# Performance work log

Hardware: AMD Instinct MI355X
Metric: run time of the kernel (lower is better)

The kernel has to match this reference:

```python
import jax, jax.numpy as jnp
import numpy as np

N = 30000      # nodes
E = 480000     # edges (before self loops)
C = 64         # in_channels
L = 32         # latent_dim
H = 2          # heads
SLOPE = 0.2    # PyG GATConv default negative_slope


def _param(key, shape, fan_in):
    return jax.random.normal(key, shape, jnp.float32) * (1.0 / np.sqrt(fan_in))


def setup_inputs() -> dict:
    key = jax.random.key(0)
    ks = jax.random.split(key, 32)
    d = {
        "x": jax.random.normal(ks[0], (N, C), jnp.float32),
        "edge_index": jax.random.randint(ks[1], (2, E), 0, N),
        "use_neighbors": 1,
        # GATConv params: W [heads*out, in], att_src/att_dst [heads, out], bias [heads*out]
        # encoder_conv1: in=C, out=2C, heads=H
        "W1": _param(ks[2], (H * 2 * C, C), C),
        "as1": _param(ks[3], (H, 2 * C), 2 * C),
        "ad1": _param(ks[4], (H, 2 * C), 2 * C),
        "b1": jnp.zeros((H * 2 * C,), jnp.float32),
        # encoder_conv2: in=2C*H, out=L, heads=1
        "W2": _param(ks[5], (L, 2 * C * H), 2 * C * H),
        "as2": _param(ks[6], (1, L), L),
        "ad2": _param(ks[7], (1, L), L),
        "b2": jnp.zeros((L,), jnp.float32),
        # decoder_conv1: in=L, out=2C, heads=H
        "W3": _param(ks[8], (H * 2 * C, L), L),
        "as3": _param(ks[9], (H, 2 * C), 2 * C),
        "ad3": _param(ks[10], (H, 2 * C), 2 * C),
        "b3": jnp.zeros((H * 2 * C,), jnp.float32),
        # decoder_conv2: in=2C*H, out=C, heads=1
        "W4": _param(ks[11], (C, 2 * C * H), 2 * C * H),
        "as4": _param(ks[12], (1, C), C),
        "ad4": _param(ks[13], (1, C), C),
        "b4": jnp.zeros((C,), jnp.float32),
        # dense (non-neighbor) branch Linear params [out, in] + bias
        "el1w": _param(ks[14], (2 * C, C), C), "el1b": jnp.zeros((2 * C,), jnp.float32),
        "el2w": _param(ks[15], (L, 2 * C), 2 * C), "el2b": jnp.zeros((L,), jnp.float32),
        "dl1w": _param(ks[16], (2 * C, L), L), "dl1b": jnp.zeros((2 * C,), jnp.float32),
        "dl2w": _param(ks[17], (C, 2 * C), 2 * C), "dl2b": jnp.zeros((C,), jnp.float32),
    }
    return d


def gat_conv(x, src, dst, W, att_src, att_dst, bias, heads, out_ch):
    """PyG GATConv (concat=True, self loops already in src/dst)."""
    n = x.shape[0]
    h = (x @ W.T).reshape(n, heads, out_ch)            # [N,H,F]
    a_s = jnp.sum(h * att_src[None], -1)               # [N,H]
    a_d = jnp.sum(h * att_dst[None], -1)               # [N,H]
    e = jax.nn.leaky_relu(a_s[src] + a_d[dst], SLOPE)  # [Etot,H]
    m = jax.ops.segment_max(e, dst, num_segments=n)
    ex = jnp.exp(e - m[dst])
    den = jax.ops.segment_sum(ex, dst, num_segments=n)
    alpha = ex / den[dst]                              # segment softmax over incoming edges
    msg = h[src] * alpha[..., None]                    # [Etot,H,F]
    out = jax.ops.segment_sum(msg, dst, num_segments=n)
    return out.reshape(n, heads * out_ch) + bias


def reference(x, edge_index, use_neighbors,
              W1, as1, ad1, b1, W2, as2, ad2, b2,
              W3, as3, ad3, b3, W4, as4, ad4, b4,
              el1w, el1b, el2w, el2b, dl1w, dl1b, dl2w, dl2b):
    if use_neighbors:
        loops = jnp.arange(N)
        src = jnp.concatenate([edge_index[0], loops])
        dst = jnp.concatenate([edge_index[1], loops])
        h = jax.nn.relu(gat_conv(x, src, dst, W1, as1, ad1, b1, H, 2 * C))
        z = gat_conv(h, src, dst, W2, as2, ad2, b2, 1, L)
        h = jax.nn.relu(gat_conv(z, src, dst, W3, as3, ad3, b3, H, 2 * C))
        return gat_conv(h, src, dst, W4, as4, ad4, b4, 1, C)
    else:
        h = jax.nn.relu(x @ el1w.T + el1b)
        z = h @ el2w.T + el2b
        h = jax.nn.relu(z @ dl1w.T + dl1b)
        return h @ dl2w.T + dl2b
```

## Files before the change

### kernel.cpp

```cpp
#include <hip/hip_runtime.h>
#include <hip/hip_bf16.h>
#include <math.h>

#define NODES 30000
#define WAVE 64
#define SCAN_T 1024
#define SCAN_CH 32
#define SCAN_CAP (SCAN_T * SCAN_CH)

static __device__ __forceinline__ float lrelu(float x) {
    return (x > 0.f) ? x : 0.2f * x;
}

__global__ __launch_bounds__(256) void gemm_xwt(
    const float* __restrict__ X, int lda, const float* __restrict__ W,
    const float* __restrict__ bias, float* __restrict__ out, int ldc,
    int Nrows, int M, int K, int relu,
    const float* __restrict__ att_s, const float* __restrict__ att_d,
    float* __restrict__ as_out, float* __restrict__ ad_out,
    const int* __restrict__ flag, int wantFlag)
{
    if (((*flag != 0) ? 1 : 0) != wantFlag) return;

    const int z = blockIdx.z;
    X += (size_t)z * K;
    W += (size_t)z * M * K;
    if (bias) bias += (size_t)z * M;
    out += (size_t)z * M;

    __shared__ float As[16][68];
    __shared__ float Bs[16][68];

    const int t  = threadIdx.x;
    const int tx = t & 15;
    const int ty = t >> 4;
    const int rowBase = blockIdx.y * 64;
    const int colBase = blockIdx.x * 64;

    float acc[4][4];
#pragma unroll
    for (int i = 0; i < 4; i++)
#pragma unroll
        for (int j = 0; j < 4; j++) acc[i][j] = 0.f;

    const int r_ld = t >> 2;
    const int k_ld = (t & 3) * 4;

    for (int kt = 0; kt < K; kt += 16) {
        float4 av = make_float4(0.f, 0.f, 0.f, 0.f);
        int grow = rowBase + r_ld;
        if (grow < Nrows)
            av = *reinterpret_cast<const float4*>(&X[(size_t)grow * lda + kt + k_ld]);
        As[k_ld + 0][r_ld] = av.x;
        As[k_ld + 1][r_ld] = av.y;
        As[k_ld + 2][r_ld] = av.z;
        As[k_ld + 3][r_ld] = av.w;
        float4 bv = make_float4(0.f, 0.f, 0.f, 0.f);
        int gm = colBase + r_ld;
        if (gm < M)
            bv = *reinterpret_cast<const float4*>(&W[(size_t)gm * K + kt + k_ld]);
        Bs[k_ld + 0][r_ld] = bv.x;
        Bs[k_ld + 1][r_ld] = bv.y;
        Bs[k_ld + 2][r_ld] = bv.z;
        Bs[k_ld + 3][r_ld] = bv.w;
        __syncthreads();

#pragma unroll
        for (int kk = 0; kk < 16; ++kk) {
            const float4 a = *reinterpret_cast<const float4*>(&As[kk][ty * 4]);
            const float4 b = *reinterpret_cast<const float4*>(&Bs[kk][tx * 4]);
            acc[0][0] += a.x * b.x; acc[0][1] += a.x * b.y; acc[0][2] += a.x * b.z; acc[0][3] += a.x * b.w;
            acc[1][0] += a.y * b.x; acc[1][1] += a.y * b.y; acc[1][2] += a.y * b.z; acc[1][3] += a.y * b.w;
            acc[2][0] += a.z * b.x; acc[2][1] += a.z * b.y; acc[2][2] += a.z * b.z; acc[2][3] += a.z * b.w;
            acc[3][0] += a.w * b.x; acc[3][1] += a.w * b.y; acc[3][2] += a.w * b.z; acc[3][3] += a.w * b.w;
        }
        __syncthreads();
    }

    const int col0 = colBase + tx * 4;
#pragma unroll
    for (int i = 0; i < 4; i++) {
        int row = rowBase + ty * 4 + i;
        if (row >= Nrows) continue;
        if (col0 >= M) continue;
        float4 v = make_float4(acc[i][0], acc[i][1], acc[i][2], acc[i][3]);
        if (bias) {
            v.x += bias[col0 + 0]; v.y += bias[col0 + 1];
            v.z += bias[col0 + 2]; v.w += bias[col0 + 3];
        }
        if (relu) {
            v.x = fmaxf(v.x, 0.f); v.y = fmaxf(v.y, 0.f);
            v.z = fmaxf(v.z, 0.f); v.w = fmaxf(v.w, 0.f);
        }
        *reinterpret_cast<float4*>(&out[(size_t)row * ldc + col0]) = v;
    }

    if (att_s) {
        float4 asv = make_float4(0.f, 0.f, 0.f, 0.f), adv = asv;
        if (col0 < M) {
            asv = *reinterpret_cast<const float4*>(&att_s[col0]);
            adv = *reinterpret_cast<const float4*>(&att_d[col0]);
        }
#pragma unroll
        for (int i = 0; i < 4; i++) {
            float ps = acc[i][0] * asv.x + acc[i][1] * asv.y + acc[i][2] * asv.z + acc[i][3] * asv.w;
            float pd = acc[i][0] * adv.x + acc[i][1] * adv.y + acc[i][2] * adv.z + acc[i][3] * adv.w;
#pragma unroll
            for (int off = 8; off; off >>= 1) {
                ps += __shfl_xor(ps, off);
                pd += __shfl_xor(pd, off);
            }
            int row = rowBase + ty * 4 + i;
            if (tx == 0 && row < Nrows) {
                as_out[row] = ps;
                ad_out[row] = pd;
            }
        }
    }
}

template <int HH, int F, int K>
__global__ __launch_bounds__(256) void fold_att(
    const float* __restrict__ W, const float* __restrict__ as_,
    const float* __restrict__ ad_, float* __restrict__ us,
    float* __restrict__ ud, const int* __restrict__ flag)
{
    if (*flag == 0) return;
    const int b   = blockIdx.x;
    const int sel = b / HH;
    const int h   = b % HH;
    const float* att = sel ? ad_ : as_;
    float* uo = sel ? ud : us;

    constexpr int NG = 256 / K;
    const int k  = threadIdx.x % K;
    const int fg = threadIdx.x / K;

    float s = 0.f;
#pragma unroll
    for (int f = fg; f < F; f += NG)
        s += att[h * F + f] * W[(size_t)(h * F + f) * K + k];

    __shared__ float red[256];
    red[threadIdx.x] = s;
    __syncthreads();
    if (fg == 0) {
        float tot = s;
#pragma unroll
        for (int g = 1; g < NG; g++) tot += red[g * K + k];
        uo[h * K + k] = tot;
    }
}

template <int K, int HH>
__global__ __launch_bounds__(256) void att_from_x(
    const float* __restrict__ xin, const float* __restrict__ us,
    const float* __restrict__ ud, float* __restrict__ as_out,
    float* __restrict__ ad_out, const int* __restrict__ flag)
{
    if (*flag == 0) return;
    constexpr int NPW = WAVE / K;
    const int wid  = threadIdx.x >> 6;
    const int lane = threadIdx.x & 63;
    const int sub  = lane / K;
    const int col  = lane % K;
    const int node = (blockIdx.x * 4 + wid) * NPW + sub;

    float v = 0.f;
    if (node < NODES) v = xin[(size_t)node * K + col];
    float ps[HH], pd[HH];
#pragma unroll
    for (int h = 0; h < HH; h++) {
        ps[h] = v * us[h * K + col];
        pd[h] = v * ud[h * K + col];
    }
#pragma unroll
    for (int off = K / 2; off; off >>= 1) {
#pragma unroll
        for (int h = 0; h < HH; h++) {
            ps[h] += __shfl_xor(ps[h], off);
            pd[h] += __shfl_xor(pd[h], off);
        }
    }
    if (col == 0 && node < NODES) {
#pragma unroll
        for (int h = 0; h < HH; h++) {
            as_out[node * HH + h] = ps[h];
            ad_out[node * HH + h] = pd[h];
        }
    }
}

template <int K, int HH>
__global__ __launch_bounds__(256) void gat_aggr_x(
    const float* __restrict__ xin, const float* __restrict__ as_,
    const float* __restrict__ ad_, const int* __restrict__ rowptr,
    const int* __restrict__ csr_src, float* __restrict__ agg,
    const int* __restrict__ flag)
{
    if (*flag == 0) return;
    const int node = blockIdx.x * 4 + (threadIdx.x >> 6);
    const int lane = threadIdx.x & 63;
    if (node >= NODES) return;

    const int beg = rowptr[node], end = rowptr[node + 1];
    const int deg = end - beg;

    float adv[HH];
#pragma unroll
    for (int h = 0; h < HH; h++) adv[h] = ad_[node * HH + h];

    float wl[HH];
    float mx[HH], rden[HH];
    const bool fast = (deg <= WAVE);

    if (fast) {
        float e[HH];
        int i = beg + lane;
        if (i < end) {
            int s = csr_src[i];
#pragma unroll
            for (int h = 0; h < HH; h++)
                e[h] = lrelu(as_[s * HH + h] + adv[h]);
        } else {
#pragma unroll
            for (int h = 0; h < HH; h++) e[h] = -1e30f;
        }
#pragma unroll
        for (int h = 0; h < HH; h++) {
            mx[h] = e[h];
#pragma unroll
            for (int off = 32; off; off >>= 1)
                mx[h] = fmaxf(mx[h], __shfl_xor(mx[h], off));
            float ex = __expf(e[h] - mx[h]);
            wl[h] = ex;
            float dn = ex;
#pragma unroll
            for (int off = 32; off; off >>= 1)
                dn += __shfl_xor(dn, off);
            rden[h] = 1.f / dn;
        }
    } else {
        float den[HH];
#pragma unroll
        for (int h = 0; h < HH; h++) { mx[h] = -1e30f; den[h] = 0.f; }
        for (int i = beg + lane; i < end; i += WAVE) {
            int s = csr_src[i];
#pragma unroll
            for (int h = 0; h < HH; h++)
                mx[h] = fmaxf(mx[h], lrelu(as_[s * HH + h] + adv[h]));
        }
#pragma unroll
        for (int h = 0; h < HH; h++)
#pragma unroll
            for (int off = 32; off; off >>= 1)
                mx[h] = fmaxf(mx[h], __shfl_xor(mx[h], off));
        for (int i = beg + lane; i < end; i += WAVE) {
            int s = csr_src[i];
#pragma unroll
            for (int h = 0; h < HH; h++)
                den[h] += __expf(lrelu(as_[s * HH + h] + adv[h]) - mx[h]);
        }
#pragma unroll
        for (int h = 0; h < HH; h++) {
#pragma unroll
            for (int off = 32; off; off >>= 1)
                den[h] += __shfl_xor(den[h], off);
            rden[h] = 1.f / den[h];
        }
    }

    constexpr int LPG = K / 4;
    constexpr int GR  = WAVE / LPG;
    const int esub = lane / LPG;
    const int c4   = lane % LPG;

    float4 acc[HH];
#pragma unroll
    for (int h = 0; h < HH; h++) acc[h] = make_float4(0.f, 0.f, 0.f, 0.f);

    if (fast) {
        const int iters = (deg + GR - 1) / GR;
        for (int it = 0; it < iters; ++it) {
            const int i = beg + it * GR + esub;
            const bool valid = (i < end);
            const int srcl = valid ? (i - beg) : 0;
            float w[HH];
#pragma unroll
            for (int h = 0; h < HH; h++)
                w[h] = __shfl(wl[h], srcl);
            if (valid) {
                int s = csr_src[i];
                float4 xv = *reinterpret_cast<const float4*>(&xin[(size_t)s * K + c4 * 4]);
#pragma unroll
                for (int h = 0; h < HH; h++) {
                    acc[h].x += xv.x * w[h];
                    acc[h].y += xv.y * w[h];
                    acc[h].z += xv.z * w[h];
                    acc[h].w += xv.w * w[h];
                }
            }
        }
    } else {
        for (int i = beg + esub; i < end; i += GR) {
            int s = csr_src[i];
            float w[HH];
#pragma unroll
            for (int h = 0; h < HH; h++)
                w[h] = __expf(lrelu(as_[s * HH + h] + adv[h]) - mx[h]);
            float4 xv = *reinterpret_cast<const float4*>(&xin[(size_t)s * K + c4 * 4]);
#pragma unroll
            for (int h = 0; h < HH; h++) {
                acc[h].x += xv.x * w[h];
                acc[h].y += xv.y * w[h];
                acc[h].z += xv.z * w[h];
                acc[h].w += xv.w * w[h];
            }
        }
    }
#pragma unroll
    for (int off = LPG; off < WAVE; off <<= 1) {
#pragma unroll
        for (int h = 0; h < HH; h++) {
            acc[h].x += __shfl_xor(acc[h].x, off);
            acc[h].y += __shfl_xor(acc[h].y, off);
            acc[h].z += __shfl_xor(acc[h].z, off);
            acc[h].w += __shfl_xor(acc[h].w, off);
        }
    }
    if (esub == 0) {
#pragma unroll
        for (int h = 0; h < HH; h++) {
            float4 o = make_float4(acc[h].x * rden[h], acc[h].y * rden[h],
                                   acc[h].z * rden[h], acc[h].w * rden[h]);
            *reinterpret_cast<float4*>(&agg[(size_t)node * (HH * K) + h * K + c4 * 4]) = o;
        }
    }
}

template <int HF, int RELU>
__global__ __launch_bounds__(256) void gat_aggr_h(
    const float* __restrict__ hsrc, const float* __restrict__ as_,
    const float* __restrict__ ad_, const int* __restrict__ rowptr,
    const int* __restrict__ csr_src, const float* __restrict__ bias,
    float* __restrict__ out, const int* __restrict__ flag)
{
    if (*flag == 0) return;
    const int node = blockIdx.x * 4 + (threadIdx.x >> 6);
    const int lane = threadIdx.x & 63;
    if (node >= NODES) return;

    const int beg = rowptr[node], end = rowptr[node + 1];
    const int deg = end - beg;
    const float adv = ad_[node];

    float wl, mx, rden;
    const bool fast = (deg <= WAVE);

    if (fast) {
        int i = beg + lane;
        float e = -1e30f;
        if (i < end) {
            int s = csr_src[i];
            e = lrelu(as_[s] + adv);
        }
        mx = e;
#pragma unroll
        for (int off = 32; off; off >>= 1)
            mx = fmaxf(mx, __shfl_xor(mx, off));
        wl = __expf(e - mx);
        float dn = wl;
#pragma unroll
        for (int off = 32; off; off >>= 1)
            dn += __shfl_xor(dn, off);
        rden = 1.f / dn;
    } else {
        mx = -1e30f;
        float den = 0.f;
        for (int i = beg + lane; i < end; i += WAVE) {
            int s = csr_src[i];
            mx = fmaxf(mx, lrelu(as_[s] + adv));
        }
#pragma unroll
        for (int off = 32; off; off >>= 1)
            mx = fmaxf(mx, __shfl_xor(mx, off));
        for (int i = beg + lane; i < end; i += WAVE) {
            int s = csr_src[i];
            den += __expf(lrelu(as_[s] + adv) - mx);
        }
#pragma unroll
        for (int off = 32; off; off >>= 1)
            den += __shfl_xor(den, off);
        rden = 1.f / den;
        wl = 0.f;
    }

    constexpr int LPG = HF / 4;
    constexpr int GR  = WAVE / LPG;
    const int esub = lane / LPG;
    const int c4   = lane % LPG;

    float4 acc = make_float4(0.f, 0.f, 0.f, 0.f);
    if (fast) {
        const int iters = (deg + GR - 1) / GR;
        for (int it = 0; it < iters; ++it) {
            const int i = beg + it * GR + esub;
            const bool valid = (i < end);
            const int srcl = valid ? (i - beg) : 0;
            float w = __shfl(wl, srcl);
            if (valid) {
                int s = csr_src[i];
                float4 hv = *reinterpret_cast<const float4*>(&hsrc[(size_t)s * HF + c4 * 4]);
                acc.x += hv.x * w; acc.y += hv.y * w; acc.z += hv.z * w; acc.w += hv.w * w;
            }
        }
    } else {
        for (int i = beg + esub; i < end; i += GR) {
            int s = csr_src[i];
            float w = __expf(lrelu(as_[s] + adv) - mx);
            float4 hv = *reinterpret_cast<const float4*>(&hsrc[(size_t)s * HF + c4 * 4]);
            acc.x += hv.x * w; acc.y += hv.y * w; acc.z += hv.z * w; acc.w += hv.w * w;
        }
    }
#pragma unroll
    for (int off = LPG; off < WAVE; off <<= 1) {
        acc.x += __shfl_xor(acc.x, off);
        acc.y += __shfl_xor(acc.y, off);
        acc.z += __shfl_xor(acc.z, off);
        acc.w += __shfl_xor(acc.w, off);
    }
    if (esub == 0) {
        float4 bv = *reinterpret_cast<const float4*>(&bias[c4 * 4]);
        float4 o = make_float4(acc.x * rden + bv.x, acc.y * rden + bv.y,
                               acc.z * rden + bv.z, acc.w * rden + bv.w);
        if (RELU) {
            o.x = fmaxf(o.x, 0.f); o.y = fmaxf(o.y, 0.f);
            o.z = fmaxf(o.z, 0.f); o.w = fmaxf(o.w, 0.f);
        }
        *reinterpret_cast<float4*>(&out[(size_t)node * HF + c4 * 4]) = o;
    }
}

__global__ void zero_int(int* __restrict__ p, int n, const int* __restrict__ flag)
{
    if (*flag == 0) return;
    for (int i = blockIdx.x * blockDim.x + threadIdx.x; i < n; i += gridDim.x * blockDim.x)
        p[i] = 0;
}

__global__ void count_deg(const int* __restrict__ ei, int* __restrict__ deg,
                          int E_, int Nn, const int* __restrict__ flag)
{
    if (*flag == 0) return;
    int e = blockIdx.x * blockDim.x + threadIdx.x;
    int tot = E_ + Nn;
    if (e >= tot) return;
    int dst = (e < E_) ? ei[E_ + e] : (e - E_);
    atomicAdd(&deg[dst], 1);
}

__global__ __launch_bounds__(SCAN_T) void scan_deg(
    const int* __restrict__ deg, int* __restrict__ rowptr,
    int* __restrict__ cursor, const int* __restrict__ flag)
{
    if (*flag == 0) return;
    __shared__ int sums[SCAN_T];
    const int t = threadIdx.x;
    const int base = t * SCAN_CH;

    int v[SCAN_CH];
    const int4* dp = reinterpret_cast<const int4*>(deg + base);
#pragma unroll
    for (int j = 0; j < SCAN_CH / 4; j++) {
        int4 q = dp[j];
        v[4 * j + 0] = q.x; v[4 * j + 1] = q.y;
        v[4 * j + 2] = q.z; v[4 * j + 3] = q.w;
    }
    int s = 0;
#pragma unroll
    for (int j = 0; j < SCAN_CH; j++) s += v[j];
    sums[t] = s;
    __syncthreads();
    for (int off = 1; off < SCAN_T; off <<= 1) {
        int x = (t >= off) ? sums[t - off] : 0;
        __syncthreads();
        sums[t] += x;
        __syncthreads();
    }
    int run = sums[t] - s;
    if (t == 0) rowptr[0] = 0;
#pragma unroll
    for (int j = 0; j < SCAN_CH; j++) {
        cursor[base + j] = run;
        run += v[j];
        rowptr[base + j + 1] = run;
    }
}

__global__ void scatter_edges(const int* __restrict__ ei, int* __restrict__ cursor,
                              int* __restrict__ csr_src, int E_, int Nn,
                              const int* __restrict__ flag)
{
    if (*flag == 0) return;
    int e = blockIdx.x * blockDim.x + threadIdx.x;
    int tot = E_ + Nn;
    if (e >= tot) return;
    int src, dst;
    if (e < E_) { src = ei[e]; dst = ei[E_ + e]; }
    else        { src = e - E_; dst = src; }
    int pos = atomicAdd(&cursor[dst], 1);
    csr_src[pos] = src;
}

extern "C" void kernel_launch(void* const* d_in, const int* in_sizes, int n_in,
                              void* d_out, int out_size, void* d_ws, size_t ws_size,
                              hipStream_t stream)
{
    const float* x    = (const float*)d_in[0];
    const int*   ei   = (const int*)d_in[1];
    const int*   flag = (const int*)d_in[2];
    const float* W1 = (const float*)d_in[3];
    const float* as1 = (const float*)d_in[4];
    const float* ad1 = (const float*)d_in[5];
    const float* b1 = (const float*)d_in[6];
    const float* W2 = (const float*)d_in[7];
    const float* as2 = (const float*)d_in[8];
    const float* ad2 = (const float*)d_in[9];
    const float* b2 = (const float*)d_in[10];
    const float* W3 = (const float*)d_in[11];
    const float* as3 = (const float*)d_in[12];
    const float* ad3 = (const float*)d_in[13];
    const float* b3 = (const float*)d_in[14];
    const float* W4 = (const float*)d_in[15];
    const float* as4 = (const float*)d_in[16];
    const float* ad4 = (const float*)d_in[17];
    const float* b4 = (const float*)d_in[18];
    const float* el1w = (const float*)d_in[19];
    const float* el1b = (const float*)d_in[20];
    const float* el2w = (const float*)d_in[21];
    const float* el2b = (const float*)d_in[22];
    const float* dl1w = (const float*)d_in[23];
    const float* dl1b = (const float*)d_in[24];
    const float* dl2w = (const float*)d_in[25];
    const float* dl2b = (const float*)d_in[26];

    const int E_   = in_sizes[1] / 2;
    const int Etot = E_ + NODES;

    char* base = (char*)d_ws;
    size_t off = 0;
    auto carve = [&](size_t bytes) -> void* {
        void* p = base + off;
        off = (off + bytes + 255) & ~(size_t)255;
        return p;
    };
    float* T0  = (float*)carve((size_t)NODES * 128 * 4);
    float* A   = (float*)carve((size_t)NODES * 256 * 4);
    float* T1  = (float*)carve((size_t)NODES * 64 * 4);
    float* Bz  = (float*)carve((size_t)NODES * 32 * 4);
    float* asb = (float*)carve((size_t)NODES * 2 * 4);
    float* adb = (float*)carve((size_t)NODES * 2 * 4);
    float* u1s = (float*)carve(2 * 64 * 4);
    float* u1d = (float*)carve(2 * 64 * 4);
    float* u3s = (float*)carve(2 * 32 * 4);
    float* u3d = (float*)carve(2 * 32 * 4);
    int* deg    = (int*)carve((size_t)SCAN_CAP * 4);
    int* rowptr = (int*)carve((size_t)(SCAN_CAP + 1) * 4);
    int* cursor = (int*)carve((size_t)SCAN_CAP * 4);
    int* csr    = (int*)carve((size_t)Etot * 4);
    (void)ws_size; (void)n_in; (void)out_size;

    float* outp = (float*)d_out;
    float* agg  = T0;

    const int nodeBlocks = (NODES + 3) / 4;
    const int edgeBlocks = (Etot + 255) / 256;
    dim3 blk(256);
    const int rowTiles = (NODES + 63) / 64;

    zero_int<<<(SCAN_CAP + 255) / 256, 256, 0, stream>>>(deg, SCAN_CAP, flag);
    count_deg<<<edgeBlocks, 256, 0, stream>>>(ei, deg, E_, NODES, flag);
    scan_deg<<<1, SCAN_T, 0, stream>>>(deg, rowptr, cursor, flag);
    scatter_edges<<<edgeBlocks, 256, 0, stream>>>(ei, cursor, csr, E_, NODES, flag);

    fold_att<2, 128, 64><<<4, 256, 0, stream>>>(W1, as1, ad1, u1s, u1d, flag);
    att_from_x<64, 2><<<nodeBlocks, blk, 0, stream>>>(x, u1s, u1d, asb, adb, flag);
    gat_aggr_x<64, 2><<<nodeBlocks, blk, 0, stream>>>(x, asb, adb, rowptr, csr, agg, flag);
    gemm_xwt<<<dim3(2, rowTiles, 2), blk, 0, stream>>>(agg, 128, W1, b1, A, 256, NODES, 128, 64, 1,
                                                       nullptr, nullptr, nullptr, nullptr, flag, 1);

    gemm_xwt<<<dim3(1, rowTiles, 1), blk, 0, stream>>>(A, 256, W2, nullptr, T1, 32, NODES, 32, 256, 0,
                                                       as2, ad2, asb, adb, flag, 1);
    gat_aggr_h<32, 0><<<nodeBlocks, blk, 0, stream>>>(T1, asb, adb, rowptr, csr, b2, Bz, flag);

    fold_att<2, 128, 32><<<4, 256, 0, stream>>>(W3, as3, ad3, u3s, u3d, flag);
    att_from_x<32, 2><<<(NODES + 7) / 8, blk, 0, stream>>>(Bz, u3s, u3d, asb, adb, flag);
    gat_aggr_x<32, 2><<<nodeBlocks, blk, 0, stream>>>(Bz, asb, adb, rowptr, csr, agg, flag);
    gemm_xwt<<<dim3(2, rowTiles, 2), blk, 0, stream>>>(agg, 64, W3, b3, A, 256, NODES, 128, 32, 1,
                                                       nullptr, nullptr, nullptr, nullptr, flag, 1);

    gemm_xwt<<<dim3(1, rowTiles, 1), blk, 0, stream>>>(A, 256, W4, nullptr, T1, 64, NODES, 64, 256, 0,
                                                       as4, ad4, asb, adb, flag, 1);
    gat_aggr_h<64, 0><<<nodeBlocks, blk, 0, stream>>>(T1, asb, adb, rowptr, csr, b4, outp, flag);

    gemm_xwt<<<dim3(2, rowTiles, 1), blk, 0, stream>>>(x,  64,  el1w, el1b, T0,   128, NODES, 128, 64, 1,
                                                       nullptr, nullptr, nullptr, nullptr, flag, 0);
    gemm_xwt<<<dim3(1, rowTiles, 1), blk, 0, stream>>>(T0, 128, el2w, el2b, Bz,   32,  NODES, 32, 128, 0,
                                                       nullptr, nullptr, nullptr, nullptr, flag, 0);
    gemm_xwt<<<dim3(2, rowTiles, 1), blk, 0, stream>>>(Bz, 32,  dl1w, dl1b, A,    128, NODES, 128, 32, 1,
                                                       nullptr, nullptr, nullptr, nullptr, flag, 0);
    gemm_xwt<<<dim3(1, rowTiles, 1), blk, 0, stream>>>(A,  128, dl2w, dl2b, outp, 64,  NODES, 64, 128, 0,
                                                       nullptr, nullptr, nullptr, nullptr, flag, 0);
}
```

Baseline: 383.3 us.

## Run GAT layer GEMMs on bf16 MFMA with bf16 intermediates

Replaces the four fp32 tiled GEMMs on the neighbor path with a bf16 MFMA kernel (16x16x32). Weights are converted to bf16 each call, and the aggregation and first-GEMM outputs are stored as bf16 to halve traffic. Attention dot products are accumulated with atomics after zeroing buffers. Lowers precision to bf16 and adds conversion and zeroing launches.

```diff
diff --git a/kernel.cpp b/kernel.cpp
--- a/kernel.cpp
+++ b/kernel.cpp
@@ -8,16 +8,99 @@
 #define SCAN_CH 32
 #define SCAN_CAP (SCAN_T * SCAN_CH)
 
+typedef __attribute__((ext_vector_type(8))) short short8b;
+typedef __attribute__((ext_vector_type(4))) float floatx4;
+
 static __device__ __forceinline__ float lrelu(float x) {
     return (x > 0.f) ? x : 0.2f * x;
+}
+
+static __device__ __forceinline__ unsigned short f2bf(float f) {
+    union { float f; unsigned u; } v; v.f = f;
+    unsigned r = v.u + 0x7FFF + ((v.u >> 16) & 1);
+    return (unsigned short)(r >> 16);
+}
+
+template <int K, int M, int OUT_BF16, int RELU, int DOTS>
+__global__ __launch_bounds__(256) void gemm_mfma(
+    const unsigned short* __restrict__ Xb, int ldx,
+    const unsigned short* __restrict__ Wb,
+    const float* __restrict__ bias,
+    void* __restrict__ outv, int ldc,
+    const float* __restrict__ att_s, const float* __restrict__ att_d,
+    float* __restrict__ as_out, float* __restrict__ ad_out,
+    const int* __restrict__ flag, int Nrows)
+{
+    if (*flag == 0) return;
+    constexpr int KC = K / 32;
+    const int w    = threadIdx.x >> 6;
+    const int lane = threadIdx.x & 63;
+    const int z    = blockIdx.z;
+    const int ct   = blockIdx.y;
+    const int rowBase = blockIdx.x * 64 + w * 16;
+
+    const int lr = lane & 15;
+    const int lk = (lane >> 4) * 8;
+
+    const int arow = min(rowBase + lr, Nrows - 1);
+    const unsigned short* ap = Xb + (size_t)arow * ldx + z * K + lk;
+    short8b a[KC];
+#pragma unroll
+    for (int kc = 0; kc < KC; kc++)
+        a[kc] = *reinterpret_cast<const short8b*>(ap + kc * 32);
+
+    const unsigned short* bp = Wb + (size_t)(z * M + ct * 16 + lr) * K + lk;
+    short8b b[KC];
+#pragma unroll
+    for (int kc = 0; kc < KC; kc++)
+        b[kc] = *reinterpret_cast<const short8b*>(bp + kc * 32);
+
+    floatx4 c = {0.f, 0.f, 0.f, 0.f};
+#pragma unroll
+    for (int kc = 0; kc < KC; kc++)
+        c = __builtin_amdgcn_mfma_f32_16x16x32_bf16(a[kc], b[kc], c, 0, 0, 0);
+
+    const int colg = z * M + ct * 16 + lr;
+    const float bv = bias ? bias[colg] : 0.f;
+
+#pragma unroll
+    for (int i = 0; i < 4; i++) {
+        int r = rowBase + (lane >> 4) * 4 + i;
+        float v = c[i] + bv;
+        if (RELU) v = fmaxf(v, 0.f);
+        if (r < Nrows) {
+            if (OUT_BF16)
+                ((unsigned short*)outv)[(size_t)r * ldc + colg] = f2bf(v);
+            else
+                ((float*)outv)[(size_t)r * ldc + colg] = v;
+        }
+    }
+
+    if (DOTS) {
+        const float as_v = att_s[colg];
+        const float ad_v = att_d[colg];
+#pragma unroll
+        for (int i = 0; i < 4; i++) {
+            int r = rowBase + (lane >> 4) * 4 + i;
+            float ps = c[i] * as_v;
+            float pd = c[i] * ad_v;
+#pragma unroll
+            for (int off = 8; off; off >>= 1) {
+                ps += __shfl_xor(ps, off);
+                pd += __shfl_xor(pd, off);
+            }
+            if (lr == 0 && r < Nrows) {
+                atomicAdd(&as_out[r], ps);
+                atomicAdd(&ad_out[r], pd);
+            }
+        }
+    }
 }
 
 __global__ __launch_bounds__(256) void gemm_xwt(
     const float* __restrict__ X, int lda, const float* __restrict__ W,
     const float* __restrict__ bias, float* __restrict__ out, int ldc,
     int Nrows, int M, int K, int relu,
-    const float* __restrict__ att_s, const float* __restrict__ att_d,
-    float* __restrict__ as_out, float* __restrict__ ad_out,
     const int* __restrict__ flag, int wantFlag)
 {
     if (((*flag != 0) ? 1 : 0) != wantFlag) return;
@@ -77,11 +160,11 @@
         __syncthreads();
     }
 
-    const int col0 = colBase + tx * 4;
 #pragma unroll
     for (int i = 0; i < 4; i++) {
         int row = rowBase + ty * 4 + i;
         if (row >= Nrows) continue;
+        int col0 = colBase + tx * 4;
         if (col0 >= M) continue;
         float4 v = make_float4(acc[i][0], acc[i][1], acc[i][2], acc[i][3]);
         if (bias) {
@@ -94,29 +177,31 @@
         }
         *reinterpret_cast<float4*>(&out[(size_t)row * ldc + col0]) = v;
     }
-
-    if (att_s) {
-        float4 asv = make_float4(0.f, 0.f, 0.f, 0.f), adv = asv;
-        if (col0 < M) {
-            asv = *reinterpret_cast<const float4*>(&att_s[col0]);
-            adv = *reinterpret_cast<const float4*>(&att_d[col0]);
-        }
-#pragma unroll
-        for (int i = 0; i < 4; i++) {
-            float ps = acc[i][0] * asv.x + acc[i][1] * asv.y + acc[i][2] * asv.z + acc[i][3] * asv.w;
-            float pd = acc[i][0] * adv.x + acc[i][1] * adv.y + acc[i][2] * adv.z + acc[i][3] * adv.w;
-#pragma unroll
-            for (int off = 8; off; off >>= 1) {
-                ps += __shfl_xor(ps, off);
-                pd += __shfl_xor(pd, off);
-            }
-            int row = rowBase + ty * 4 + i;
-            if (tx == 0 && row < Nrows) {
-                as_out[row] = ps;
-                ad_out[row] = pd;
-            }
-        }
-    }
+}
+
+__global__ void cvt_bf16(const float* __restrict__ s0, unsigned short* __restrict__ d0, int n0,
+                         const float* __restrict__ s1, unsigned short* __restrict__ d1, int n1,
+                         const float* __restrict__ s2, unsigned short* __restrict__ d2, int n2,
+                         const float* __restrict__ s3, unsigned short* __restrict__ d3, int n3,
+                         const int* __restrict__ flag)
+{
+    if (*flag == 0) return;
+    int i = blockIdx.x * blockDim.x + threadIdx.x;
+    if (i < n0) { d0[i] = f2bf(s0[i]); return; }
+    i -= n0;
+    if (i < n1) { d1[i] = f2bf(s1[i]); return; }
+    i -= n1;
+    if (i < n2) { d2[i] = f2bf(s2[i]); return; }
+    i -= n2;
+    if (i < n3) d3[i] = f2bf(s3[i]);
+}
+
+__global__ void zero_f2(float* __restrict__ a, float* __restrict__ b, int n,
+                        const int* __restrict__ flag)
+{
+    if (*flag == 0) return;
+    int i = blockIdx.x * blockDim.x + threadIdx.x;
+    if (i < n) { a[i] = 0.f; b[i] = 0.f; }
 }
 
 template <int HH, int F, int K>
@@ -195,7 +280,7 @@
 __global__ __launch_bounds__(256) void gat_aggr_x(
     const float* __restrict__ xin, const float* __restrict__ as_,
     const float* __restrict__ ad_, const int* __restrict__ rowptr,
-    const int* __restrict__ csr_src, float* __restrict__ agg,
+    const int* __restrict__ csr_src, unsigned short* __restrict__ aggb,
     const int* __restrict__ flag)
 {
     if (*flag == 0) return;
@@ -331,9 +416,12 @@
     if (esub == 0) {
 #pragma unroll
         for (int h = 0; h < HH; h++) {
-            float4 o = make_float4(acc[h].x * rden[h], acc[h].y * rden[h],
-                                   acc[h].z * rden[h], acc[h].w * rden[h]);
-            *reinterpret_cast<float4*>(&agg[(size_t)node * (HH * K) + h * K + c4 * 4]) = o;
+            ushort4 o;
+            o.x = f2bf(acc[h].x * rden[h]);
+            o.y = f2bf(acc[h].y * rden[h]);
+            o.z = f2bf(acc[h].z * rden[h]);
+            o.w = f2bf(acc[h].w * rden[h]);
+            *reinterpret_cast<ushort4*>(&aggb[(size_t)node * (HH * K) + h * K + c4 * 4]) = o;
         }
     }
 }
@@ -564,6 +652,12 @@
     float* u1d = (float*)carve(2 * 64 * 4);
     float* u3s = (float*)carve(2 * 32 * 4);
     float* u3d = (float*)carve(2 * 32 * 4);
+    unsigned short* aggb = (unsigned short*)carve((size_t)NODES * 128 * 2);
+    unsigned short* Ab   = (unsigned short*)carve((size_t)NODES * 256 * 2);
+    unsigned short* wb1  = (unsigned short*)carve(256 * 64 * 2);
+    unsigned short* wb2  = (unsigned short*)carve(32 * 256 * 2);
+    unsigned short* wb3  = (unsigned short*)carve(256 * 32 * 2);
+    unsigned short* wb4  = (unsigned short*)carve(64 * 256 * 2);
     int* deg    = (int*)carve((size_t)SCAN_CAP * 4);
     int* rowptr = (int*)carve((size_t)(SCAN_CAP + 1) * 4);
     int* cursor = (int*)carve((size_t)SCAN_CAP * 4);
@@ -571,7 +665,6 @@
     (void)ws_size; (void)n_in; (void)out_size;
 
     float* outp = (float*)d_out;
-    float* agg  = T0;
 
     const int nodeBlocks = (NODES + 3) / 4;
     const int edgeBlocks = (Etot + 255) / 256;
@@ -582,33 +675,33 @@
     count_deg<<<edgeBlocks, 256, 0, stream>>>(ei, deg, E_, NODES, flag);
     scan_deg<<<1, SCAN_T, 0, stream>>>(deg, rowptr, cursor, flag);
     scatter_edges<<<edgeBlocks, 256, 0, stream>>>(ei, cursor, csr, E_, NODES, flag);
+    cvt_bf16<<<(16384 + 8192 + 8192 + 16384 + 255) / 256, 256, 0, stream>>>(
+        W1, wb1, 16384, W2, wb2, 8192, W3, wb3, 8192, W4, wb4, 16384, flag);
 
     fold_att<2, 128, 64><<<4, 256, 0, stream>>>(W1, as1, ad1, u1s, u1d, flag);
     att_from_x<64, 2><<<nodeBlocks, blk, 0, stream>>>(x, u1s, u1d, asb, adb, flag);
-    gat_aggr_x<64, 2><<<nodeBlocks, blk, 0, stream>>>(x, asb, adb, rowptr, csr, agg, flag);
-    gemm_xwt<<<dim3(2, rowTiles, 2), blk, 0, stream>>>(agg, 128, W1, b1, A, 256, NODES, 128, 64, 1,
-                                                       nullptr, nullptr, nullptr, nullptr, flag, 1);
-
-    gemm_xwt<<<dim3(1, rowTiles, 1), blk, 0, stream>>>(A, 256, W2, nullptr, T1, 32, NODES, 32, 256, 0,
-                                                       as2, ad2, asb, adb, flag, 1);
+    gat_aggr_x<64, 2><<<nodeBlocks, blk, 0, stream>>>(x, asb, adb, rowptr, csr, aggb, flag);
+    gemm_mfma<64, 128, 1, 1, 0><<<dim3(rowTiles, 8, 2), blk, 0, stream>>>(
+        aggb, 128, wb1, b1, Ab, 256, nullptr, nullptr, nullptr, nullptr, flag, NODES);
+
+    zero_f2<<<(NODES + 255) / 256, 256, 0, stream>>>(asb, adb, NODES, flag);
+    gemm_mfma<256, 32, 0, 0, 1><<<dim3(rowTiles, 2, 1), blk, 0, stream>>>(
+        Ab, 256, wb2, nullptr, T1, 32, as2, ad2, asb, adb, flag, NODES);
     gat_aggr_h<32, 0><<<nodeBlocks, blk, 0, stream>>>(T1, asb, adb, rowptr, csr, b2, Bz, flag);
 
     fold_att<2, 128, 32><<<4, 256, 0, stream>>>(W3, as3, ad3, u3s, u3d, flag);
     att_from_x<32, 2><<<(NODES + 7) / 8, blk, 0, stream>>>(Bz, u3s, u3d, asb, adb, flag);
-    gat_aggr_x<32, 2><<<nodeBlocks, blk, 0, stream>>>(Bz, asb, adb, rowptr, csr, agg, flag);
-    gemm_xwt<<<dim3(2, rowTiles, 2), blk, 0, stream>>>(agg, 64, W3, b3, A, 256, NODES, 128, 32, 1,
-                                                       nullptr, nullptr, nullptr, nullptr, flag, 1);
-
-    gemm_xwt<<<dim3(1, rowTiles, 1), blk, 0, stream>>>(A, 256, W4, nullptr, T1, 64, NODES, 64, 256, 0,
-                                                       as4, ad4, asb, adb, flag, 1);
+    gat_aggr_x<32, 2><<<nodeBlocks, blk, 0, stream>>>(Bz, asb, adb, rowptr, csr, aggb, flag);
+    gemm_mfma<32, 128, 1, 1, 0><<<dim3(rowTiles, 8, 2), blk, 0, stream>>>(
+        aggb, 64, wb3, b3, Ab, 256, nullptr, nullptr, nullptr, nullptr, flag, NODES);
+
+    zero_f2<<<(NODES + 255) / 256, 256, 0, stream>>>(asb, adb, NODES, flag);
+    gemm_mfma<256, 64, 0, 0, 1><<<dim3(rowTiles, 4, 1), blk, 0, stream>>>(
+        Ab, 256, wb4, nullptr, T1, 64, as4, ad4, asb, adb, flag, NODES);
     gat_aggr_h<64, 0><<<nodeBlocks, blk, 0, stream>>>(T1, asb, adb, rowptr, csr, b4, outp, flag);
 
-    gemm_xwt<<<dim3(2, rowTiles, 1), blk, 0, stream>>>(x,  64,  el1w, el1b, T0,   128, NODES, 128, 64, 1,
-                                                       nullptr, nullptr, nullptr, nullptr, flag, 0);
-    gemm_xwt<<<dim3(1, rowTiles, 1), blk, 0, stream>>>(T0, 128, el2w, el2b, Bz,   32,  NODES, 32, 128, 0,
-                                                       nullptr, nullptr, nullptr, nullptr, flag, 0);
-    gemm_xwt<<<dim3(2, rowTiles, 1), blk, 0, stream>>>(Bz, 32,  dl1w, dl1b, A,    128, NODES, 128, 32, 1,
-                                                       nullptr, nullptr, nullptr, nullptr, flag, 0);
-    gemm_xwt<<<dim3(1, rowTiles, 1), blk, 0, stream>>>(A,  128, dl2w, dl2b, outp, 64,  NODES, 64, 128, 0,
-                                                       nullptr, nullptr, nullptr, nullptr, flag, 0);
-}
+    gemm_xwt<<<dim3(2, rowTiles, 1), blk, 0, stream>>>(x,  64,  el1w, el1b, T0,   128, NODES, 128, 64, 1, flag, 0);
+    gemm_xwt<<<dim3(1, rowTiles, 1), blk, 0, stream>>>(T0, 128, el2w, el2b, Bz,   32,  NODES, 32, 128, 0, flag, 0);
+    gemm_xwt<<<dim3(2, rowTiles, 1), blk, 0, stream>>>(Bz, 32,  dl1w, dl1b, A,    128, NODES, 128, 32, 1, flag, 0);
+    gemm_xwt<<<dim3(1, rowTiles, 1), blk, 0, stream>>>(A,  128, dl2w, dl2b, outp, 64,  NODES, 64, 128, 0, flag, 0);
+}
```

Measured after the change: 383.9 us. About the same (+0.2%).
